# Kernel optimization log

Hardware: AMD Instinct MI355X
Metric: run time of the kernel (lower is better)

Reference implementation:

```python
import jax, jax.numpy as jnp
import numpy as np


def setup_inputs() -> dict:
    key = jax.random.key(0)
    B, C, H, W = 32, 128, 112, 112
    inp = jax.random.normal(key, (B, C, H, W), dtype=jnp.float32)
    # binomial blur filter for filt_size=4: outer([1,3,3,1]) normalized, repeated per channel
    a = np.array([1.0, 3.0, 3.0, 1.0])
    f = a[:, None] * a[None, :]
    f = f / f.sum()
    filt = jnp.asarray(np.broadcast_to(f[None, None], (C, 1, 4, 4)).copy(), dtype=jnp.float32)
    return {"inp": inp, "filt": filt}


def _polyphase_select_l2(x):
    # x: [B,C,H,W] with even H,W (aps_pad is a no-op). Returns [B] int index in {0..3}.
    p0 = x[:, :, 0::2, 0::2]
    p1 = x[:, :, 1::2, 0::2]
    p2 = x[:, :, 0::2, 1::2]
    p3 = x[:, :, 1::2, 1::2]
    norms = jnp.stack(
        [jnp.sqrt(jnp.sum(p * p, axis=(1, 2, 3))) for p in (p0, p1, p2, p3)], axis=1
    )  # [B,4]
    return jnp.argmax(norms, axis=1)


def reference(inp, filt):
    # 1) per-sample polyphase component selection on the raw input (criterion 'l2')
    idx = _polyphase_select_l2(inp)  # [B]
    C = inp.shape[1]
    # 2) reflect pad (left=1, right=2, top=1, bottom=2 for filt_size=4) + depthwise blur
    xp = jnp.pad(inp, ((0, 0), (0, 0), (1, 2), (1, 2)), mode='reflect')
    blurred = jax.lax.conv_general_dilated(
        xp, filt, window_strides=(1, 1), padding='VALID',
        dimension_numbers=('NCHW', 'OIHW', 'NCHW'), feature_group_count=C)
    # 3) stride-2 polyphase downsample selecting the chosen phase per sample
    p0 = blurred[:, :, 0::2, 0::2]
    p1 = blurred[:, :, 1::2, 0::2]
    p2 = blurred[:, :, 0::2, 1::2]
    p3 = blurred[:, :, 1::2, 1::2]
    poly = jnp.stack([p0, p1, p2, p3], axis=1)  # [B,4,C,H/2,W/2]
    out = jnp.take_along_axis(poly, idx[:, None, None, None, None], axis=1)[:, 0]
    return out  # [B,C,H/2,W/2]
```

## Files before the change

### kernel.cpp

```cpp
#include <hip/hip_runtime.h>

#define HW_   12544
#define W_    112
#define C_    128
#define OHW_  3136
#define OW_   56

__global__ __launch_bounds__(256) void phase_norms(const float* __restrict__ inp,
                                                   float* __restrict__ sums) {
    const int b = blockIdx.y;
    const float4* src = (const float4*)(inp + (size_t)b * (C_ * HW_));
    const unsigned tid = threadIdx.x;
    const unsigned base = blockIdx.x * 4096u + tid;

    float s[4] = {0.f, 0.f, 0.f, 0.f};
#pragma unroll
    for (int k = 0; k < 16; ++k) {
        unsigned g = base + k * 256u;
        float4 v = src[g];
        unsigned hp = (g / 28u) & 1u;
        s[hp]      += v.x * v.x + v.z * v.z;
        s[hp + 2u] += v.y * v.y + v.w * v.w;
    }

#pragma unroll
    for (int p = 0; p < 4; ++p) {
        float v = s[p];
        for (int off = 32; off > 0; off >>= 1) v += __shfl_down(v, off);
        s[p] = v;
    }

    __shared__ float bs[4];
    if (tid < 4) bs[tid] = 0.f;
    __syncthreads();
    if ((tid & 63u) == 0u) {
#pragma unroll
        for (int p = 0; p < 4; ++p) atomicAdd(&bs[p], s[p]);
    }
    __syncthreads();
    if (tid < 4) atomicAdd(&sums[b * 4 + tid], bs[tid]);
}

__global__ __launch_bounds__(256) void blur_select(const float* __restrict__ inp,
                                                   const float* __restrict__ sums,
                                                   float* __restrict__ out) {
    __shared__ float tile[HW_];
    const int bc = blockIdx.x;
    const int b  = bc >> 7;
    const float4* src = (const float4*)(inp + (size_t)bc * HW_);
    float4* t4 = (float4*)tile;
    for (int i = threadIdx.x; i < HW_ / 4; i += 256) t4[i] = src[i];

    const float n0 = sums[b * 4 + 0], n1 = sums[b * 4 + 1];
    const float n2 = sums[b * 4 + 2], n3 = sums[b * 4 + 3];
    int idx = 0; float best = n0;
    if (n1 > best) { best = n1; idx = 1; }
    if (n2 > best) { best = n2; idx = 2; }
    if (n3 > best) { best = n3; idx = 3; }
    const int dr = idx & 1, dc = idx >> 1;

    __syncthreads();

    float* o = out + (size_t)bc * OHW_;
    for (unsigned t = threadIdx.x; t < OHW_; t += 256) {
        const int oh = t / OW_;
        const int ow = t - oh * OW_;
        const int rb = oh * 2 + dr - 1;
        const int cb = ow * 2 + dc - 1;
        int r[4], c[4];
#pragma unroll
        for (int k = 0; k < 4; ++k) {
            int j  = rb + k;
            r[k] = (j  < 0 ? -j  : (j  > 111 ? 222 - j  : j)) * W_;
            int jc = cb + k;
            c[k] = (jc < 0 ? -jc : (jc > 111 ? 222 - jc : jc));
        }
        float acc = 0.f;
#pragma unroll
        for (int kh = 0; kh < 4; ++kh) {
            const float w = (kh == 1 || kh == 2) ? 3.f : 1.f;
            const float h = tile[r[kh] + c[0]] + 3.f * tile[r[kh] + c[1]]
                          + 3.f * tile[r[kh] + c[2]] + tile[r[kh] + c[3]];
            acc += w * h;
        }
        o[t] = acc * 0.015625f;
    }
}

extern "C" void kernel_launch(void* const* d_in, const int* in_sizes, int n_in,
                              void* d_out, int out_size, void* d_ws, size_t ws_size,
                              hipStream_t stream) {
    const float* inp = (const float*)d_in[0];
    float* sums = (float*)d_ws;
    hipMemsetAsync(d_ws, 0, 32 * 4 * sizeof(float), stream);
    phase_norms<<<dim3(98, 32), 256, 0, stream>>>(inp, sums);
    blur_select<<<4096, 256, 0, stream>>>(inp, sums, (float*)d_out);
}
```

Before: 95.27 us.

## Drop LDS staging in blur, compute 7 outputs per thread, replace atomics with partials

The phase-norm kernel now writes per-block partial sums to workspace instead of using atomics, which removes the memset launch. The blur kernel reduces those partials itself. It no longer stages the whole 112x112 plane in 50KB of LDS; each of 448 threads reads its input directly from global memory and computes 7 adjacent outputs in registers, reusing the horizontal taps across them. This should raise occupancy and skip the LDS copy and barrier. The cost is more global/L2 reads with a strided, uncoalesced pattern and higher register pressure.

```diff
diff --git a/kernel.cpp b/kernel.cpp
--- a/kernel.cpp
+++ b/kernel.cpp
@@ -1,13 +1,14 @@
 #include <hip/hip_runtime.h>
 
-#define HW_   12544
-#define W_    112
-#define C_    128
-#define OHW_  3136
-#define OW_   56
+#define HW_    12544
+#define W_     112
+#define C_     128
+#define OHW_   3136
+#define OW_    56
+#define NCHUNK 98
 
 __global__ __launch_bounds__(256) void phase_norms(const float* __restrict__ inp,
-                                                   float* __restrict__ sums) {
+                                                   float* __restrict__ part) {
     const int b = blockIdx.y;
     const float4* src = (const float4*)(inp + (size_t)b * (C_ * HW_));
     const unsigned tid = threadIdx.x;
@@ -30,69 +31,91 @@
         s[p] = v;
     }
 
-    __shared__ float bs[4];
-    if (tid < 4) bs[tid] = 0.f;
-    __syncthreads();
+    __shared__ float bs[4][4];
+    const unsigned wid = tid >> 6;
     if ((tid & 63u) == 0u) {
 #pragma unroll
-        for (int p = 0; p < 4; ++p) atomicAdd(&bs[p], s[p]);
+        for (int p = 0; p < 4; ++p) bs[wid][p] = s[p];
     }
     __syncthreads();
-    if (tid < 4) atomicAdd(&sums[b * 4 + tid], bs[tid]);
+    if (tid < 4) {
+        float v = bs[0][tid] + bs[1][tid] + bs[2][tid] + bs[3][tid];
+        part[((size_t)b * NCHUNK + blockIdx.x) * 4 + tid] = v;
+    }
 }
 
-__global__ __launch_bounds__(256) void blur_select(const float* __restrict__ inp,
-                                                   const float* __restrict__ sums,
+__global__ __launch_bounds__(448) void blur_select(const float* __restrict__ inp,
+                                                   const float* __restrict__ part,
                                                    float* __restrict__ out) {
-    __shared__ float tile[HW_];
     const int bc = blockIdx.x;
     const int b  = bc >> 7;
-    const float4* src = (const float4*)(inp + (size_t)bc * HW_);
-    float4* t4 = (float4*)tile;
-    for (int i = threadIdx.x; i < HW_ / 4; i += 256) t4[i] = src[i];
+    const int t  = threadIdx.x;
 
-    const float n0 = sums[b * 4 + 0], n1 = sums[b * 4 + 1];
-    const float n2 = sums[b * 4 + 2], n3 = sums[b * 4 + 3];
+    __shared__ float s4[4];
+    {
+        const int wid = t >> 6, lane = t & 63;
+        if (wid < 4) {
+            const float* pp = part + (size_t)b * NCHUNK * 4 + wid;
+            float v = (lane < NCHUNK) ? pp[lane * 4] : 0.f;
+            if (lane + 64 < NCHUNK) v += pp[(lane + 64) * 4];
+            for (int off = 32; off > 0; off >>= 1) v += __shfl_down(v, off);
+            if (lane == 0) s4[wid] = v;
+        }
+    }
+    __syncthreads();
+    const float n0 = s4[0], n1 = s4[1], n2 = s4[2], n3 = s4[3];
     int idx = 0; float best = n0;
     if (n1 > best) { best = n1; idx = 1; }
     if (n2 > best) { best = n2; idx = 2; }
     if (n3 > best) { best = n3; idx = 3; }
     const int dr = idx & 1, dc = idx >> 1;
 
-    __syncthreads();
+    const int oh  = t >> 3;
+    const int st  = t & 7;
+    const int ow0 = st * 7;
+    const float* P = inp + (size_t)bc * HW_;
 
-    float* o = out + (size_t)bc * OHW_;
-    for (unsigned t = threadIdx.x; t < OHW_; t += 256) {
-        const int oh = t / OW_;
-        const int ow = t - oh * OW_;
-        const int rb = oh * 2 + dr - 1;
-        const int cb = ow * 2 + dc - 1;
-        int r[4], c[4];
+    const float* rows[4];
+    const int rb = oh * 2 + dr - 1;
 #pragma unroll
-        for (int k = 0; k < 4; ++k) {
-            int j  = rb + k;
-            r[k] = (j  < 0 ? -j  : (j  > 111 ? 222 - j  : j)) * W_;
-            int jc = cb + k;
-            c[k] = (jc < 0 ? -jc : (jc > 111 ? 222 - jc : jc));
-        }
-        float acc = 0.f;
+    for (int k = 0; k < 4; ++k) {
+        int j = rb + k;
+        int aj = j < 0 ? -j : j;
+        j = min(aj, 222 - aj);
+        rows[k] = P + j * W_;
+    }
+
+    int cidx[16];
+    const int cb = ow0 * 2 + dc - 1;
 #pragma unroll
-        for (int kh = 0; kh < 4; ++kh) {
-            const float w = (kh == 1 || kh == 2) ? 3.f : 1.f;
-            const float h = tile[r[kh] + c[0]] + 3.f * tile[r[kh] + c[1]]
-                          + 3.f * tile[r[kh] + c[2]] + tile[r[kh] + c[3]];
-            acc += w * h;
-        }
-        o[t] = acc * 0.015625f;
+    for (int m = 0; m < 16; ++m) {
+        int j = cb + m;
+        int aj = j < 0 ? -j : j;
+        cidx[m] = min(aj, 222 - aj);
     }
+
+    float h[4][7];
+#pragma unroll
+    for (int k = 0; k < 4; ++k) {
+        float x[16];
+#pragma unroll
+        for (int m = 0; m < 16; ++m) x[m] = rows[k][cidx[m]];
+#pragma unroll
+        for (int j = 0; j < 7; ++j)
+            h[k][j] = (x[2*j] + x[2*j+3]) + 3.f * (x[2*j+1] + x[2*j+2]);
+    }
+
+    float* o = out + (size_t)bc * OHW_ + oh * OW_ + ow0;
+#pragma unroll
+    for (int j = 0; j < 7; ++j)
+        o[j] = ((h[0][j] + h[3][j]) + 3.f * (h[1][j] + h[2][j])) * 0.015625f;
 }
 
 extern "C" void kernel_launch(void* const* d_in, const int* in_sizes, int n_in,
                               void* d_out, int out_size, void* d_ws, size_t ws_size,
                               hipStream_t stream) {
     const float* inp = (const float*)d_in[0];
-    float* sums = (float*)d_ws;
-    hipMemsetAsync(d_ws, 0, 32 * 4 * sizeof(float), stream);
-    phase_norms<<<dim3(98, 32), 256, 0, stream>>>(inp, sums);
-    blur_select<<<4096, 256, 0, stream>>>(inp, sums, (float*)d_out);
+    float* part = (float*)d_ws;
+    phase_norms<<<dim3(NCHUNK, 32), 256, 0, stream>>>(inp, part);
+    blur_select<<<4096, 448, 0, stream>>>(inp, part, (float*)d_out);
 }
```

New measurement: 155.5 us. 1.63x slower.
